# Kernel optimization log

Hardware: AMD Instinct MI355X
Metric: run time of the kernel (lower is better)

## Reference

```python
import jax, jax.numpy as jnp
import numpy as np

B, S, BERT_H = 8, 512, 432
NL, HD = 12, 64
H = NL * HD  # 768
NEG = -1e12

def _lin(k, i, o):
    return jax.random.normal(k, (i, o), jnp.float32) * 0.02

def setup_inputs():
    key = jax.random.key(0)
    ks = jax.random.split(key, 12)
    return {
        "bert_hidden": jax.random.normal(ks[0], (B, S, BERT_H), jnp.float32),
        "attention_mask": jnp.ones((B, S), jnp.float32),
        "dense_w": _lin(ks[1], BERT_H, H), "dense_b": jnp.zeros((H,)),
        "sat_qw": _lin(ks[2], H, H), "sat_qb": jnp.zeros((H,)),
        "sat_kw": _lin(ks[3], H, H), "sat_kb": jnp.zeros((H,)),
        "sat_vw": _lin(ks[4], H, H), "sat_vb": jnp.zeros((H,)),
        "sat_ow": _lin(ks[5], H, H), "sat_ob": jnp.zeros((H,)),
        "rel_qw": _lin(ks[6], H, H), "rel_qb": jnp.zeros((H,)),
        "rel_kw": _lin(ks[7], H, H), "rel_kb": jnp.zeros((H,)),
        "rel_vw": _lin(ks[8], H, H), "rel_vb": jnp.zeros((H,)),
        "rel_ow": _lin(ks[9], H, H), "rel_ob": jnp.zeros((H,)),
        "lns_w": jnp.ones((H,)), "lns_b": jnp.zeros((H,)),
        "lnr_w": jnp.ones((H,)), "lnr_b": jnp.zeros((H,)),
        "head_w": _lin(ks[10], H, 2 * HD), "head_b": jnp.zeros((2 * HD,)),
        "tail_w": _lin(ks[11], 2 * HD, 2 * NL), "tail_b": jnp.zeros((2 * NL,)),
    }

def _layernorm(x, w, b, eps=1e-12):
    u = x.mean(-1, keepdims=True)
    s = ((x - u) ** 2).mean(-1, keepdims=True)
    return w * (x - u) / jnp.sqrt(s + eps) + b

def _mha(q_in, k_in, v_in, wq, bq, wk, bk, wv, bv, wo, bo):
    # q_in: [N, Lq, H]; k_in/v_in: [N, Lk, H]; dropout is identity (eval)
    N, Lq, _ = q_in.shape
    Lk = k_in.shape[1]
    qh = (q_in @ wq + bq).reshape(N, Lq, NL, HD)
    kh = (k_in @ wk + bk).reshape(N, Lk, NL, HD)
    vh = (v_in @ wv + bv).reshape(N, Lk, NL, HD)
    scores = jnp.einsum('nqhd,nkhd->nhqk', qh, kh) / np.float32(np.sqrt(HD))
    probs = jax.nn.softmax(scores, axis=-1)
    ctx = jnp.einsum('nhqk,nkhd->nqhd', probs, vh).reshape(N, Lq, NL * HD)
    return ctx @ wo + bo + q_in

def _shift_back(x):
    # faithful torch cycle_shift(forward=False): circular roll left by 1
    return jnp.roll(x, -1, axis=1)

def _shift_fwd(x):
    # faithful to the torch sequential in-place loop in cycle_shift(forward=True):
    # out[0] = x[-1]; out[1:] = x[0] (each copy reads the already-overwritten slot)
    b, s, h = x.shape
    return jnp.concatenate([x[:, -1:, :], jnp.broadcast_to(x[:, :1, :], (b, s - 1, h))], axis=1)

def reference(bert_hidden, attention_mask, dense_w, dense_b,
              sat_qw, sat_qb, sat_kw, sat_kb, sat_vw, sat_vb, sat_ow, sat_ob,
              rel_qw, rel_qb, rel_kw, rel_kb, rel_vw, rel_vb, rel_ow, rel_ob,
              lns_w, lns_b, lnr_w, lnr_b, head_w, head_b, tail_w, tail_b):
    hidden0 = bert_hidden @ dense_w + dense_b  # [B,S,H]
    cs = hidden0
    center = cs.mean(axis=1)  # [B,H], avg_pool2d over seq dim
    for _ in range(2):
        before = _shift_back(cs)
        after = _shift_fwd(cs)
        center_exp = jnp.broadcast_to(center[:, None, :], cs.shape)
        concats = jnp.stack([before, cs, after, hidden0, center_exp], axis=2)  # [B,S,5,H]
        concats = concats.reshape(B * S, 5, H)
        q = cs.reshape(B * S, 1, H)
        sat = _mha(q, concats, concats, sat_qw, sat_qb, sat_kw, sat_kb, sat_vw, sat_vb, sat_ow, sat_ob)
        cs = _layernorm(jax.nn.relu(sat), lns_w, lns_b).reshape(B, S, H)
        cc = jnp.concatenate([center[:, None, :], cs], axis=1)  # [B,S+1,H]
        rel = _mha(center[:, None, :], cc, cc, rel_qw, rel_qb, rel_kw, rel_kb, rel_vw, rel_vb, rel_ow, rel_ob)
        center = _layernorm(jax.nn.relu(rel), lnr_w, lnr_b)[:, 0, :]
    outputs = cs @ head_w + head_b  # [B,S,2*HD]
    qw, kw = outputs[..., ::2], outputs[..., 1::2]  # [B,S,HD]
    pos = jnp.arange(S, dtype=jnp.float32)
    inv = jnp.power(10000.0, -2.0 * jnp.arange(HD // 2, dtype=jnp.float32) / HD)
    ang = pos[:, None] * inv[None, :]  # [S,HD//2]
    pe = jnp.stack([jnp.sin(ang), jnp.cos(ang)], axis=-1).reshape(S, HD)
    cos_pos = jnp.repeat(pe[:, 1::2], 2, axis=-1)  # [S,HD]
    sin_pos = jnp.repeat(pe[:, ::2], 2, axis=-1)
    def rot(x):
        x2 = jnp.stack([-x[..., 1::2], x[..., ::2]], axis=-1).reshape(x.shape)
        return x * cos_pos + x2 * sin_pos
    qw, kw = rot(qw), rot(kw)
    logits = jnp.einsum('bmd,bnd->bmn', qw, kw) / np.float32(np.sqrt(HD))  # [B,S,S]
    bias = jnp.einsum('bnh->bhn', outputs @ tail_w + tail_b) / 2.0  # [B,2*NL,S]
    logits = logits[:, None, :, :] + bias[:, ::2, None, :] + bias[:, 1::2, :, None]  # [B,NL,S,S]
    m1 = attention_mask[:, None, :, None]
    logits = logits * m1 + NEG * (1.0 - m1)
    m2 = attention_mask[:, None, None, :]
    logits = logits * m2 + NEG * (1.0 - m2)
    tril = jnp.tril(jnp.ones((S, S), logits.dtype), k=-1)
    return logits - tril * 1e12
```

## Files before the change

kernel.cpp:

```cpp
#include <hip/hip_runtime.h>
#include <cstdint>
#include <cstddef>

#define HH 768
#define SS 512
#define NBATCH 8
#define NLH 12
#define HDIM 64
#define BSROWS 4096
static constexpr float NEGV = -1000000000000.0f;

typedef unsigned short ushort_t;
typedef __attribute__((ext_vector_type(4))) float fx4;
typedef __attribute__((ext_vector_type(8))) short sx8;

__device__ __forceinline__ ushort_t f2bf(float f) {
  uint32_t u = __float_as_uint(f);
  uint32_t r = (u + 0x7FFFu + ((u >> 16) & 1u)) >> 16;
  return (ushort_t)r;
}
__device__ __forceinline__ float bf2f(ushort_t h) {
  return __uint_as_float(((uint32_t)h) << 16);
}
__device__ __forceinline__ float2 ldbf2(const ushort_t* p) {
  uint32_t u = *(const uint32_t*)p;
  return make_float2(__uint_as_float(u << 16), __uint_as_float(u & 0xffff0000u));
}

__device__ __forceinline__ void async_copy16(void* lds, const void* g) {
  __builtin_amdgcn_global_load_lds(
      (const __attribute__((address_space(1))) void*)g,
      (__attribute__((address_space(3))) void*)lds, 16, 0, 0);
}

__global__ __launch_bounds__(256) void gemm_bf16(
    const ushort_t* __restrict__ A, int lda,
    const ushort_t* __restrict__ B, int ldb,
    const float* __restrict__ bias,
    const ushort_t* __restrict__ resb,
    ushort_t* __restrict__ Cb, int ldo,
    ushort_t* __restrict__ Cb2, int ldo2, int nsplit, int K, int nx,
    float* __restrict__ colmean)
{
  __shared__ ushort_t As[128 * 64];
  __shared__ ushort_t Bs[128 * 64];
  const int tid = threadIdx.x;
  const int nwg = gridDim.x;
  const int q = nwg >> 3;
  const int xcd = blockIdx.x & 7, sidx = blockIdx.x >> 3;
  const int swz = xcd * q + sidx;
  const int bm = (swz / nx) * 128;
  const int bn = (swz % nx) * 128;
  const int l = tid & 63;
  const int w = tid >> 6;
  const int wr = w >> 1, wc = w & 1;
  const int r8 = tid >> 3;
  const int sl = tid & 7;

  fx4 acc[4][4];
#pragma unroll
  for (int m = 0; m < 4; ++m)
#pragma unroll
    for (int n = 0; n < 4; ++n) acc[m][n] = (fx4)0.f;

  for (int k0 = 0; k0 < K; k0 += 64) {
#pragma unroll
    for (int i = 0; i < 4; ++i) {
      int row = i * 32 + r8;
      int srcs = sl ^ (row & 7);
      async_copy16((char*)As + i * 4096 + tid * 16,
                   A + (size_t)(bm + row) * lda + k0 + srcs * 8);
    }
#pragma unroll
    for (int i = 0; i < 4; ++i) {
      int row = i * 32 + r8;
      int srcs = sl ^ (row & 7);
      async_copy16((char*)Bs + i * 4096 + tid * 16,
                   B + (size_t)(bn + row) * ldb + k0 + srcs * 8);
    }
    __syncthreads();
#pragma unroll
    for (int kk = 0; kk < 2; ++kk) {
      sx8 av[4], bv[4];
      const int so = (l >> 4) + kk * 4;
#pragma unroll
      for (int m = 0; m < 4; ++m) {
        int r = wr * 64 + m * 16 + (l & 15);
        av[m] = *(const sx8*)((const char*)As + r * 128 + ((so ^ (r & 7)) * 16));
      }
#pragma unroll
      for (int n = 0; n < 4; ++n) {
        int r = wc * 64 + n * 16 + (l & 15);
        bv[n] = *(const sx8*)((const char*)Bs + r * 128 + ((so ^ (r & 7)) * 16));
      }
#pragma unroll
      for (int m = 0; m < 4; ++m)
#pragma unroll
        for (int n = 0; n < 4; ++n)
          acc[m][n] = __builtin_amdgcn_mfma_f32_16x16x32_bf16(av[m], bv[n], acc[m][n], 0, 0, 0);
    }
    __syncthreads();
  }

  const bool second = (bn >= nsplit);
  ushort_t* dst = second ? Cb2 : Cb;
  const int ld = second ? ldo2 : ldo;
  const int csub = second ? nsplit : 0;
  const int cr0 = bm + wr * 64 + (l >> 4) * 4;
  const int cc0 = bn + wc * 64 + (l & 15);
#pragma unroll
  for (int m = 0; m < 4; ++m) {
#pragma unroll
    for (int n = 0; n < 4; ++n) {
      int col = cc0 + n * 16;
      float bcol = bias[col];
#pragma unroll
      for (int j = 0; j < 4; ++j) {
        int row = cr0 + m * 16 + j;
        size_t off = (size_t)row * ld + (col - csub);
        float v = acc[m][n][j] + bcol;
        if (resb) v += bf2f(resb[off]);
        dst[off] = f2bf(v);
      }
    }
  }

  if (colmean) {
    float* scr = (float*)As;
    const int cid = wr * 4 + (l >> 4);
#pragma unroll
    for (int n = 0; n < 4; ++n) {
      int colL = wc * 64 + n * 16 + (l & 15);
      float t = 16.0f * bias[bn + colL];
#pragma unroll
      for (int m = 0; m < 4; ++m)
#pragma unroll
        for (int j = 0; j < 4; ++j) t += acc[m][n][j];
      scr[cid * 128 + colL] = t;
    }
    __syncthreads();
    if (tid < 128) {
      float scol = 0.f;
#pragma unroll
      for (int c = 0; c < 8; ++c) scol += scr[c * 128 + tid];
      atomicAdd(&colmean[(bm >> 9) * HH + bn + tid], scol * (1.0f / 512.0f));
    }
  }
}

__global__ __launch_bounds__(256) void head_fused(
    const ushort_t* __restrict__ A,
    const ushort_t* __restrict__ B,
    const float* __restrict__ head_b,
    const float* __restrict__ tail_w,
    const float* __restrict__ tail_b,
    float* __restrict__ qw, float* __restrict__ kw,
    float* __restrict__ bias2)
{
  __shared__ ushort_t As[128 * 64];
  __shared__ ushort_t Bs[128 * 64];
  __shared__ float tile[128][130];
  __shared__ float invt[32];
  const int tid = threadIdx.x;
  const int bm = blockIdx.x * 128;
  const int l = tid & 63;
  const int w = tid >> 6;
  const int wr = w >> 1, wc = w & 1;
  const int r8 = tid >> 3;
  const int sl = tid & 7;

  if (tid < 32) invt[tid] = powf(10000.0f, -(float)tid / 32.0f);

  fx4 acc[4][4];
#pragma unroll
  for (int m = 0; m < 4; ++m)
#pragma unroll
    for (int n = 0; n < 4; ++n) acc[m][n] = (fx4)0.f;

  for (int k0 = 0; k0 < HH; k0 += 64) {
#pragma unroll
    for (int i = 0; i < 4; ++i) {
      int row = i * 32 + r8;
      int srcs = sl ^ (row & 7);
      async_copy16((char*)As + i * 4096 + tid * 16,
                   A + (size_t)(bm + row) * HH + k0 + srcs * 8);
    }
#pragma unroll
    for (int i = 0; i < 4; ++i) {
      int row = i * 32 + r8;
      int srcs = sl ^ (row & 7);
      async_copy16((char*)Bs + i * 4096 + tid * 16,
                   B + (size_t)row * HH + k0 + srcs * 8);
    }
    __syncthreads();
#pragma unroll
    for (int kk = 0; kk < 2; ++kk) {
      sx8 av[4], bv[4];
      const int so = (l >> 4) + kk * 4;
#pragma unroll
      for (int m = 0; m < 4; ++m) {
        int r = wr * 64 + m * 16 + (l & 15);
        av[m] = *(const sx8*)((const char*)As + r * 128 + ((so ^ (r & 7)) * 16));
      }
#pragma unroll
      for (int n = 0; n < 4; ++n) {
        int r = wc * 64 + n * 16 + (l & 15);
        bv[n] = *(const sx8*)((const char*)Bs + r * 128 + ((so ^ (r & 7)) * 16));
      }
#pragma unroll
      for (int m = 0; m < 4; ++m)
#pragma unroll
        for (int n = 0; n < 4; ++n)
          acc[m][n] = __builtin_amdgcn_mfma_f32_16x16x32_bf16(av[m], bv[n], acc[m][n], 0, 0, 0);
    }
    __syncthreads();
  }

  const int cr0 = wr * 64 + (l >> 4) * 4;
  const int cc0 = wc * 64 + (l & 15);
#pragma unroll
  for (int m = 0; m < 4; ++m)
#pragma unroll
    for (int n = 0; n < 4; ++n) {
      int col = cc0 + n * 16;
      float bcol = head_b[col];
#pragma unroll
      for (int j = 0; j < 4; ++j)
        tile[cr0 + m * 16 + j][col] = acc[m][n][j] + bcol;
    }
  __syncthreads();

  for (int t = tid; t < 128 * 32; t += 256) {
    int r = t >> 5, i = t & 31;
    int s = (bm + r) & 511;
    float ang = (float)s * invt[i];
    float sn = sinf(ang), cn = cosf(ang);
    float q0 = tile[r][4 * i + 0], k0 = tile[r][4 * i + 1];
    float q1 = tile[r][4 * i + 2], k1 = tile[r][4 * i + 3];
    float* qp = qw + (size_t)(bm + r) * 64 + i * 2;
    float* kp = kw + (size_t)(bm + r) * 64 + i * 2;
    qp[0] = q0 * cn - q1 * sn; qp[1] = q1 * cn + q0 * sn;
    kp[0] = k0 * cn - k1 * sn; kp[1] = k1 * cn + k0 * sn;
  }
  for (int t = tid; t < 128 * 24; t += 256) {
    int r = t / 24, c = t % 24;
    float acc2 = tail_b[c];
// ... 28 lines not shown
    }
    __syncthreads();
#pragma unroll
    for (int i = 0; i < 4; ++i) {
      int n = n0 + ty + i * 8;
      int k = k0 + tx;
      if (n < jb.N && k < jb.Kpad)
        jb.dst[(size_t)(jb.rowOff + n) * jb.Kpad + k] = f2bf(t[tx][ty + i * 8]);
    }
  } else {
    const int NB = BSROWS * 448;
    const int total = NB + 3840 + NBATCH * HH;
    int start = (blockIdx.y * 24 + blockIdx.x) * 256 + threadIdx.x;
    for (int i = start; i < total; i += 24 * 24 * 256) {
      if (i < NB) {
        int r = i / 448, c = i % 448;
        pa.bert_bf[i] = (c < 432) ? f2bf(pa.bert[(size_t)r * 432 + c]) : (ushort_t)0;
      } else if (i < NB + 3840) {
        int c = i - NB;
        float v;
        if (c < 768) v = pa.rkb[c];
        else if (c < 1536) v = pa.rvb[c - 768];
        else if (c < 2304) v = pa.sqb[c - 1536];
        else if (c < 3072) v = pa.skb[c - 2304];
        else v = pa.svb[c - 3072];
        pa.b_merged[c] = v;
      } else {
        pa.center[i - NB - 3840] = 0.f;
      }
    }
  }
}

struct SmallJob { const float* W; const float* bias; const float* res; float* C; };
struct SmallJobs { SmallJob j[5]; };
__global__ __launch_bounds__(256) void gemm_skinny(
    const float* __restrict__ A, SmallJobs jobs)
{
  __shared__ float As[8 * HH];
  __shared__ float part[8 * 8 * 32];
  const int tid = threadIdx.x;
  const SmallJob job = jobs.j[blockIdx.y];
#pragma unroll
  for (int i = 0; i < 6; ++i) {
    int idx = tid * 4 + i * 1024;
    *(float4*)&As[idx] = *(const float4*)(A + idx);
  }
  __syncthreads();
  const int c = tid & 31;
  const int col = (blockIdx.x << 5) + c;
  const int ks = tid >> 5;
  const float* Wp = job.W + (size_t)(ks * 96) * HH + col;
  float acc[8] = {};
#pragma unroll 8
  for (int k = 0; k < 96; ++k) {
    float wv = Wp[(size_t)k * HH];
    const float* ap = &As[ks * 96 + k];
#pragma unroll
    for (int m = 0; m < 8; ++m)
      acc[m] = fmaf(ap[m * HH], wv, acc[m]);
  }
#pragma unroll
  for (int m = 0; m < 8; ++m)
    part[ks * 256 + m * 32 + c] = acc[m];
  __syncthreads();
  const int m = tid >> 5;
  const int c2 = tid & 31;
  float s = 0.f;
#pragma unroll
  for (int k = 0; k < 8; ++k) s += part[k * 256 + m * 32 + c2];
  const int outcol = (blockIdx.x << 5) + c2;
  float v = s + job.bias[outcol];
  if (job.res) v += job.res[(size_t)m * HH + outcol];
  job.C[(size_t)m * HH + outcol] = v;
}

struct SmallJobs2 { SmallJob j[2]; };
__global__ __launch_bounds__(256) void skinny_ln(
    const float* __restrict__ relo, const float* __restrict__ lw, const float* __restrict__ lb,
    SmallJobs2 jobs)
{
  __shared__ float As[8 * HH];
  __shared__ float part[8 * 8 * 32];
  const int tid = threadIdx.x;
  const SmallJob job = jobs.j[blockIdx.y];
#pragma unroll
  for (int i = 0; i < 6; ++i) {
    int idx = tid * 4 + i * 1024;
    *(float4*)&As[idx] = *(const float4*)(relo + idx);
  }
  __syncthreads();
  {
    const int row = tid >> 5, lc = tid & 31;
    float s = 0.f, sq = 0.f;
#pragma unroll
    for (int e = 0; e < 24; ++e) {
      float x = fmaxf(As[row * HH + lc * 24 + e], 0.f);
      s += x; sq += x * x;
    }
#pragma unroll
    for (int d = 1; d < 32; d <<= 1) { s += __shfl_xor(s, d); sq += __shfl_xor(sq, d); }
    float mean = s * (1.0f / HH);
    float var = sq * (1.0f / HH) - mean * mean;
    float rstd = rsqrtf(var + 1e-12f);
#pragma unroll
    for (int e = 0; e < 24; ++e) {
      int cc = lc * 24 + e;
      float x = fmaxf(As[row * HH + cc], 0.f);
      As[row * HH + cc] = lw[cc] * (x - mean) * rstd + lb[cc];
    }
  }
  __syncthreads();
  const int c = tid & 31;
  const int col = (blockIdx.x << 5) + c;
  const int ks = tid >> 5;
  const float* Wp = job.W + (size_t)(ks * 96) * HH + col;
  float acc[8] = {};
#pragma unroll 8
  for (int k = 0; k < 96; ++k) {
    float wv = Wp[(size_t)k * HH];
    const float* ap = &As[ks * 96 + k];
#pragma unroll
    for (int m = 0; m < 8; ++m)
      acc[m] = fmaf(ap[m * HH], wv, acc[m]);
  }
#pragma unroll
  for (int m = 0; m < 8; ++m)
    part[ks * 256 + m * 32 + c] = acc[m];
  __syncthreads();
  const int m = tid >> 5;
  const int c2 = tid & 31;
  float s2 = 0.f;
#pragma unroll
  for (int k = 0; k < 8; ++k) s2 += part[k * 256 + m * 32 + c2];
  const int outcol = (blockIdx.x << 5) + c2;
  job.C[(size_t)m * HH + outcol] = s2 + job.bias[outcol];
}

__global__ __launch_bounds__(256) void sat_attn(
    const ushort_t* __restrict__ Qc, const ushort_t* __restrict__ Kc,
    const ushort_t* __restrict__ Vc, int ldq,
    const ushort_t* __restrict__ Kh0, const ushort_t* __restrict__ Vh0, int ldh,
    const float* __restrict__ Kcen, const float* __restrict__ Vcen,
    ushort_t* __restrict__ ctxb)
{
  int i = blockIdx.x;
  int b = i >> 9, s = i & 511;
  int lane = threadIdx.x & 63;
  int wave = threadIdx.x >> 6;
  size_t rb = (size_t)(b * SS + ((s + 1) & 511));
  size_t rs = (size_t)i;
  size_t ra = (size_t)(b * SS + (s == 0 ? (SS - 1) : 0));
  size_t rc = (size_t)b * HH;
  const int half = lane >> 5;
  const int d0 = (lane & 31) * 2;
#pragma unroll
  for (int it = 0; it < 2; ++it) {
    int p = wave + 4 * it;
    if (p >= 6) break;
    int off = (2 * p + half) * HDIM + d0;
    float2 q  = ldbf2(Qc + rs * ldq + off);
    float2 kb = ldbf2(Kc + rb * ldq + off);
    float2 ks = ldbf2(Kc + rs * ldq + off);
    float2 ka = ldbf2(Kc + ra * ldq + off);
    float2 kh = ldbf2(Kh0 + rs * ldh + off);
    float2 kc = *(const float2*)(Kcen + rc + off);
    float s0 = q.x * kb.x + q.y * kb.y;
    float s1 = q.x * ks.x + q.y * ks.y;
    float s2 = q.x * ka.x + q.y * ka.y;
    float s3 = q.x * kh.x + q.y * kh.y;
    float s4 = q.x * kc.x + q.y * kc.y;
// ... 21 lines not shown
}

__global__ __launch_bounds__(256) void relu_ln_bf(
    const ushort_t* __restrict__ x, const float* __restrict__ w, const float* __restrict__ b,
    ushort_t* __restrict__ ybf)
{
  int row = blockIdx.x;
  const ushort_t* xr = x + (size_t)row * HH;
  float v[3];
  float sum = 0.f, sumsq = 0.f;
#pragma unroll
  for (int j = 0; j < 3; ++j) {
    float t = bf2f(xr[threadIdx.x + j * 256]);
    t = fmaxf(t, 0.f);
    v[j] = t;
    sum += t; sumsq += t * t;
  }
#pragma unroll
  for (int d = 1; d < 64; d <<= 1) { sum += __shfl_xor(sum, d); sumsq += __shfl_xor(sumsq, d); }
  __shared__ float ws_[4], wsq_[4];
  int wave = threadIdx.x >> 6, lane = threadIdx.x & 63;
  if (lane == 0) { ws_[wave] = sum; wsq_[wave] = sumsq; }
  __syncthreads();
  sum = ws_[0] + ws_[1] + ws_[2] + ws_[3];
  sumsq = wsq_[0] + wsq_[1] + wsq_[2] + wsq_[3];
  float mean = sum * (1.0f / HH);
  float var = sumsq * (1.0f / HH) - mean * mean;
  float rstd = rsqrtf(var + 1e-12f);
#pragma unroll
  for (int j = 0; j < 3; ++j) {
    int cidx = threadIdx.x + j * 256;
    float o = w[cidx] * (v[j] - mean) * rstd + b[cidx];
    ybf[(size_t)row * HH + cidx] = f2bf(o);
  }
}

__global__ __launch_bounds__(256) void rel_attn(
    const float* __restrict__ Qr, const float* __restrict__ Krc, const ushort_t* __restrict__ Kr,
    const float* __restrict__ Vrc, const ushort_t* __restrict__ Vr, int ldkv,
    float* __restrict__ ctx)
{
  int b = blockIdx.x, h = blockIdx.y;
  __shared__ float qs[64];
  __shared__ float sc[513];
  __shared__ float part[4][64];
  __shared__ float redm[4], redsum[4];
  int t = threadIdx.x, lane = t & 63, wave = t >> 6;
  if (t < 64) qs[t] = Qr[b * HH + h * HDIM + t];
  __syncthreads();
  for (int j = t; j < 513; j += 256) {
    float acc = 0.f;
    if (j == 0) {
      const float* kp = Krc + b * HH + h * HDIM;
#pragma unroll
      for (int d = 0; d < HDIM; ++d) acc = fmaf(qs[d], kp[d], acc);
    } else {
      const sx8* kv = (const sx8*)(Kr + (size_t)(b * SS + j - 1) * ldkv + h * HDIM);
#pragma unroll
      for (int dq = 0; dq < 8; ++dq) {
        sx8 v = kv[dq];
#pragma unroll
        for (int e = 0; e < 8; ++e)
          acc = fmaf(qs[dq * 8 + e], bf2f((ushort_t)v[e]), acc);
      }
    }
    sc[j] = acc * 0.125f;
  }
  __syncthreads();
  float m = -1e30f;
  for (int j = t; j < 513; j += 256) m = fmaxf(m, sc[j]);
#pragma unroll
  for (int d = 1; d < 64; d <<= 1) m = fmaxf(m, __shfl_xor(m, d));
  if (lane == 0) redm[wave] = m;
  __syncthreads();
  m = fmaxf(fmaxf(redm[0], redm[1]), fmaxf(redm[2], redm[3]));
  float lsum = 0.f;
  for (int j = t; j < 513; j += 256) { float e = __expf(sc[j] - m); sc[j] = e; lsum += e; }
#pragma unroll
  for (int d = 1; d < 64; d <<= 1) lsum += __shfl_xor(lsum, d);
  if (lane == 0) redsum[wave] = lsum;
  __syncthreads();
  float total = redsum[0] + redsum[1] + redsum[2] + redsum[3];
  float accv = 0.f;
#pragma unroll 8
  for (int j = wave; j < 513; j += 4) {
    float vv = (j == 0) ? Vrc[b * HH + h * HDIM + lane]
                        : bf2f(Vr[(size_t)(b * SS + j - 1) * ldkv + h * HDIM + lane]);
    accv = fmaf(sc[j], vv, accv);
  }
  part[wave][lane] = accv;
  __syncthreads();
  if (wave == 0) {
    float r = (part[0][lane] + part[1][lane] + part[2][lane] + part[3][lane]) / total;
    ctx[b * HH + h * HDIM + lane] = r;
  }
}

__global__ __launch_bounds__(256) void final_kernel(
    const float* __restrict__ qw, const float* __restrict__ kw,
    const float* __restrict__ bias2, const float* __restrict__ mask,
    float* __restrict__ out)
{
  int b = blockIdx.z;
  int mt = blockIdx.y * 32;
  int nt = blockIdx.x * 32;
  __shared__ float qs[32][68];
  __shared__ float ks[32][68];
  int t = threadIdx.x;
  {
    int idx = t * 8;
    int r = idx >> 6, c = idx & 63;
    const float* sq = qw + (size_t)(b * SS + mt + r) * 64 + c;
    const float* sk = kw + (size_t)(b * SS + nt + r) * 64 + c;
    *(float4*)&qs[r][c]     = *(const float4*)(sq);
    *(float4*)&qs[r][c + 4] = *(const float4*)(sq + 4);
    *(float4*)&ks[r][c]     = *(const float4*)(sk);
    *(float4*)&ks[r][c + 4] = *(const float4*)(sk + 4);
  }
  __syncthreads();
  int m = t >> 3;
  int n0 = (t & 7) * 4;
  float d0 = 0.f, d1 = 0.f, d2 = 0.f, d3 = 0.f;
#pragma unroll
  for (int d = 0; d < 64; d += 4) {
    float4 qv = *(const float4*)&qs[m][d];
    float4 k0 = *(const float4*)&ks[n0 + 0][d];
    float4 k1 = *(const float4*)&ks[n0 + 1][d];
// ... 60 lines not shown
  const float* rel_vw  = (const float*)d_in[16];
  const float* rel_vb  = (const float*)d_in[17];
  const float* rel_ow  = (const float*)d_in[18];
  const float* rel_ob  = (const float*)d_in[19];
  const float* lns_w   = (const float*)d_in[20];
  const float* lns_b   = (const float*)d_in[21];
  const float* lnr_w   = (const float*)d_in[22];
  const float* lnr_b   = (const float*)d_in[23];
  const float* head_w  = (const float*)d_in[24];
  const float* head_b  = (const float*)d_in[25];
  const float* tail_w  = (const float*)d_in[26];
  const float* tail_b  = (const float*)d_in[27];

  float* out = (float*)d_out;
  char*  ws  = (char*)d_ws;

  size_t off = 0;
  auto alloc = [&](size_t bytes) { char* p = ws + off; off += (bytes + 255) & ~(size_t)255; return p; };
  ushort_t* bert_bf   = (ushort_t*)alloc((size_t)BSROWS * 448 * 2);
  ushort_t* Wt_dense  = (ushort_t*)alloc((size_t)768 * 448 * 2);
  ushort_t* Wt_big    = (ushort_t*)alloc((size_t)3840 * 768 * 2);
  ushort_t* Wt_satow  = (ushort_t*)alloc((size_t)768 * 768 * 2);
  ushort_t* Wt_head   = (ushort_t*)alloc((size_t)128 * 768 * 2);
  ushort_t* hidden0_bf= (ushort_t*)alloc((size_t)BSROWS * HH * 2);
  ushort_t* ctx_bf    = (ushort_t*)alloc((size_t)BSROWS * HH * 2);
  ushort_t* csA_bf    = (ushort_t*)alloc((size_t)BSROWS * HH * 2);
  float* b_merged = (float*)alloc(3840 * 4);
  float* center   = (float*)alloc(6144 * 4);
  float* Kcen     = (float*)alloc(6144 * 4);
  float* Vcen     = (float*)alloc(6144 * 4);
  float* Qr       = (float*)alloc(6144 * 4);
  float* Krc      = (float*)alloc(6144 * 4);
  float* Vrc      = (float*)alloc(6144 * 4);
  float* ctxr     = (float*)alloc(6144 * 4);
  float* relo     = (float*)alloc(6144 * 4);
  float* bias2    = (float*)alloc((size_t)BSROWS * 24 * 4);
  float* qwbuf    = (float*)alloc((size_t)BSROWS * 64 * 4);
  float* kwbuf    = (float*)alloc((size_t)BSROWS * 64 * 4);

  ushort_t* QKV1_bf = (ushort_t*)out;
  ushort_t* tmp1_bf = QKV1_bf + (size_t)BSROWS * 2304;
  ushort_t* KrVr_bf = tmp1_bf + (size_t)BSROWS * 768;
  ushort_t* QKV2_bf = KrVr_bf + (size_t)BSROWS * 1536;
  ushort_t* tmp2_bf = tmp1_bf;

  dim3 blk(256);

  {
    PrepArgs pa;
    pa.j[0] = { dense_w, Wt_dense, 432, 768, 448, 0 };
    pa.j[1] = { rel_kw,  Wt_big,   768, 768, 768, 0 };
    pa.j[2] = { rel_vw,  Wt_big,   768, 768, 768, 768 };
    pa.j[3] = { sat_qw,  Wt_big,   768, 768, 768, 1536 };
    pa.j[4] = { sat_kw,  Wt_big,   768, 768, 768, 2304 };
    pa.j[5] = { sat_vw,  Wt_big,   768, 768, 768, 3072 };
    pa.j[6] = { sat_ow,  Wt_satow, 768, 768, 768, 0 };
    pa.j[7] = { head_w,  Wt_head,  768, 128, 768, 0 };
    pa.bert = bert; pa.bert_bf = bert_bf;
    pa.rkb = rel_kb; pa.rvb = rel_vb; pa.sqb = sat_qb; pa.skb = sat_kb; pa.svb = sat_vb;
    pa.b_merged = b_merged; pa.center = center;
    prep_all<<<dim3(24, 24, 9), blk, 0, stream>>>(pa);
  }

  gemm_bf16<<<dim3(192), blk, 0, stream>>>(bert_bf, 448, Wt_dense, 448, dense_b,
                                           nullptr, hidden0_bf, HH,
                                           nullptr, 0, 1 << 30, 448, 6, center);

  gemm_bf16<<<dim3(576), blk, 0, stream>>>(hidden0_bf, HH, Wt_big + (size_t)1536 * 768, HH,
                                           b_merged + 1536, nullptr, QKV1_bf, 2304,
                                           nullptr, 0, 1 << 30, HH, 18, nullptr);
  {
    SmallJobs jobs;
    jobs.j[0] = { sat_kw, sat_kb, nullptr, Kcen };
    jobs.j[1] = { sat_vw, sat_vb, nullptr, Vcen };
    jobs.j[2] = { rel_qw, rel_qb, nullptr, Qr };
    jobs.j[3] = { rel_kw, rel_kb, nullptr, Krc };
    jobs.j[4] = { rel_vw, rel_vb, nullptr, Vrc };
    gemm_skinny<<<dim3(24, 5), blk, 0, stream>>>(center, jobs);
  }
  sat_attn<<<BSROWS, 256, 0, stream>>>(QKV1_bf, QKV1_bf + 768, QKV1_bf + 1536, 2304,
                                       QKV1_bf + 768, QKV1_bf + 1536, 2304,
                                       Kcen, Vcen, ctx_bf);
  gemm_bf16<<<dim3(192), blk, 0, stream>>>(ctx_bf, HH, Wt_satow, HH, sat_ob,
                                           hidden0_bf, tmp1_bf, HH,
                                           nullptr, 0, 1 << 30, HH, 6, nullptr);
  relu_ln_bf<<<BSROWS, 256, 0, stream>>>(tmp1_bf, lns_w, lns_b, csA_bf);

  gemm_bf16<<<dim3(960), blk, 0, stream>>>(csA_bf, HH, Wt_big, HH, b_merged,
                                           nullptr, KrVr_bf, 1536,
                                           QKV2_bf, 2304, 1536, HH, 30, nullptr);
  rel_attn<<<dim3(8, 12), 256, 0, stream>>>(Qr, Krc, KrVr_bf, Vrc, KrVr_bf + 768, 1536, ctxr);
  {
    SmallJobs jobs;
    jobs.j[0] = { rel_ow, rel_ob, center, relo };
    gemm_skinny<<<dim3(24, 1), blk, 0, stream>>>(ctxr, jobs);
  }
  {
    SmallJobs2 jobs;
    jobs.j[0] = { sat_kw, sat_kb, nullptr, Kcen };
    jobs.j[1] = { sat_vw, sat_vb, nullptr, Vcen };
    skinny_ln<<<dim3(24, 2), blk, 0, stream>>>(relo, lnr_w, lnr_b, jobs);
  }
  sat_attn<<<BSROWS, 256, 0, stream>>>(QKV2_bf, QKV2_bf + 768, QKV2_bf + 1536, 2304,
                                       QKV1_bf + 768, QKV1_bf + 1536, 2304,
                                       Kcen, Vcen, ctx_bf);
  gemm_bf16<<<dim3(192), blk, 0, stream>>>(ctx_bf, HH, Wt_satow, HH, sat_ob,
                                           csA_bf, tmp2_bf, HH,
                                           nullptr, 0, 1 << 30, HH, 6, nullptr);
  relu_ln_bf<<<BSROWS, 256, 0, stream>>>(tmp2_bf, lns_w, lns_b, csA_bf);

  head_fused<<<32, blk, 0, stream>>>(csA_bf, Wt_head, head_b, tail_w, tail_b,
                                     qwbuf, kwbuf, bias2);
  final_kernel<<<dim3(16, 16, 8), 256, 0, stream>>>(qwbuf, kwbuf, bias2, amask, out);
}
```

Measured before the change: 311.8 us.

## Fuse small kernels: QKV GEMM with skinny jobs, relation chain, and final LN into head

Three separate fusions. The QKV1 GEMM and the skinny center projections now run in one launch with block-index dispatch. The relation attention, output projection, ReLU-LayerNorm and K/V center projections are merged into a single 1024-thread kernel per batch. The last relu_ln pass is folded into head_fused, which computes row statistics up front and normalizes the A tile while loading it. This removes several launches and intermediate round trips, but rel_fused runs on only 8 blocks with serial fp32 GEMV loops, and the head LN loads A synchronously instead of asynchronously.

```diff
diff --git a/kernel.cpp b/kernel.cpp
--- a/kernel.cpp
+++ b/kernel.cpp
@@ -31,6 +31,166 @@
   __builtin_amdgcn_global_load_lds(
       (const __attribute__((address_space(1))) void*)g,
       (__attribute__((address_space(3))) void*)lds, 16, 0, 0);
+}
+
+__device__ __forceinline__ void gemm_core(
+    char* arena, int bid, int nwg, int nx,
+    const ushort_t* __restrict__ A, int lda,
+    const ushort_t* __restrict__ B, int ldb,
+    const float* __restrict__ bias,
+    const ushort_t* __restrict__ resb,
+    ushort_t* __restrict__ Cb, int ldo,
+    ushort_t* __restrict__ Cb2, int ldo2, int nsplit, int K,
+    float* __restrict__ colmean)
+{
+  ushort_t* As = (ushort_t*)arena;
+  ushort_t* Bs = (ushort_t*)(arena + 16384);
+  const int tid = threadIdx.x;
+  const int q = nwg >> 3;
+  const int xcd = bid & 7, sidx = bid >> 3;
+  const int swz = xcd * q + sidx;
+  const int bm = (swz / nx) * 128;
+  const int bn = (swz % nx) * 128;
+  const int l = tid & 63;
+  const int w = tid >> 6;
+  const int wr = w >> 1, wc = w & 1;
+  const int r8 = tid >> 3;
+  const int sl = tid & 7;
+
+  fx4 acc[4][4];
+#pragma unroll
+  for (int m = 0; m < 4; ++m)
+#pragma unroll
+    for (int n = 0; n < 4; ++n) acc[m][n] = (fx4)0.f;
+
+  for (int k0 = 0; k0 < K; k0 += 64) {
+#pragma unroll
+    for (int i = 0; i < 4; ++i) {
+      int row = i * 32 + r8;
+      int srcs = sl ^ (row & 7);
+      async_copy16((char*)As + i * 4096 + tid * 16,
+                   A + (size_t)(bm + row) * lda + k0 + srcs * 8);
+    }
+#pragma unroll
+    for (int i = 0; i < 4; ++i) {
+      int row = i * 32 + r8;
+      int srcs = sl ^ (row & 7);
+      async_copy16((char*)Bs + i * 4096 + tid * 16,
+                   B + (size_t)(bn + row) * ldb + k0 + srcs * 8);
+    }
+    __syncthreads();
+#pragma unroll
+    for (int kk = 0; kk < 2; ++kk) {
+      sx8 av[4], bv[4];
+      const int so = (l >> 4) + kk * 4;
+#pragma unroll
+      for (int m = 0; m < 4; ++m) {
+        int r = wr * 64 + m * 16 + (l & 15);
+        av[m] = *(const sx8*)((const char*)As + r * 128 + ((so ^ (r & 7)) * 16));
+      }
+#pragma unroll
+      for (int n = 0; n < 4; ++n) {
+        int r = wc * 64 + n * 16 + (l & 15);
+        bv[n] = *(const sx8*)((const char*)Bs + r * 128 + ((so ^ (r & 7)) * 16));
+      }
+#pragma unroll
+      for (int m = 0; m < 4; ++m)
+#pragma unroll
+        for (int n = 0; n < 4; ++n)
+          acc[m][n] = __builtin_amdgcn_mfma_f32_16x16x32_bf16(av[m], bv[n], acc[m][n], 0, 0, 0);
+    }
+    __syncthreads();
+  }
+
+  const bool second = (bn >= nsplit);
+  ushort_t* dst = second ? Cb2 : Cb;
+  const int ld = second ? ldo2 : ldo;
+  const int csub = second ? nsplit : 0;
+  const int cr0 = bm + wr * 64 + (l >> 4) * 4;
+  const int cc0 = bn + wc * 64 + (l & 15);
+#pragma unroll
+  for (int m = 0; m < 4; ++m) {
+#pragma unroll
+    for (int n = 0; n < 4; ++n) {
+      int col = cc0 + n * 16;
+      float bcol = bias[col];
+#pragma unroll
+      for (int j = 0; j < 4; ++j) {
+        int row = cr0 + m * 16 + j;
+        size_t off = (size_t)row * ld + (col - csub);
+        float v = acc[m][n][j] + bcol;
+        if (resb) v += bf2f(resb[off]);
+        dst[off] = f2bf(v);
+      }
+    }
+  }
+
+  if (colmean) {
+    float* scr = (float*)arena;
+    const int cid = wr * 4 + (l >> 4);
+#pragma unroll
+    for (int n = 0; n < 4; ++n) {
+      int colL = wc * 64 + n * 16 + (l & 15);
+      float t = 16.0f * bias[bn + colL];
+#pragma unroll
+      for (int m = 0; m < 4; ++m)
+#pragma unroll
+        for (int j = 0; j < 4; ++j) t += acc[m][n][j];
+      scr[cid * 128 + colL] = t;
+    }
+    __syncthreads();
+    if (tid < 128) {
+      float scol = 0.f;
+#pragma unroll
+      for (int c = 0; c < 8; ++c) scol += scr[c * 128 + tid];
+      atomicAdd(&colmean[(bm >> 9) * HH + bn + tid], scol * (1.0f / 512.0f));
+    }
+  }
+}
+
+struct SmallJob { const float* W; const float* bias; const float* res; float* C; };
+struct SmallJobs { SmallJob j[5]; };
+
+__device__ __forceinline__ void skinny_core(
+    char* arena, int colblk,
+    const float* __restrict__ A, const float* __restrict__ W,
+    const float* __restrict__ bias, const float* __restrict__ res, float* __restrict__ C)
+{
+  float* As = (float*)arena;
+  float* part = (float*)(arena + 24576);
+  const int tid = threadIdx.x;
+#pragma unroll
+  for (int i = 0; i < 6; ++i) {
+    int idx = tid * 4 + i * 1024;
+    *(float4*)&As[idx] = *(const float4*)(A + idx);
+  }
+  __syncthreads();
+  const int c = tid & 31;
+  const int col = (colblk << 5) + c;
+  const int ks = tid >> 5;
+  const float* Wp = W + (size_t)(ks * 96) * HH + col;
+  float acc[8] = {};
+#pragma unroll 8
+  for (int k = 0; k < 96; ++k) {
+    float wv = Wp[(size_t)k * HH];
+    const float* ap = &As[ks * 96 + k];
+#pragma unroll
+    for (int m = 0; m < 8; ++m)
+      acc[m] = fmaf(ap[m * HH], wv, acc[m]);
+  }
+#pragma unroll
+  for (int m = 0; m < 8; ++m)
+    part[ks * 256 + m * 32 + c] = acc[m];
+  __syncthreads();
+  const int m = tid >> 5;
+  const int c2 = tid & 31;
+  float s = 0.f;
+#pragma unroll
+  for (int k = 0; k < 8; ++k) s += part[k * 256 + m * 32 + c2];
+  const int outcol = (colblk << 5) + c2;
+  float v = s + bias[outcol];
+  if (res) v += res[(size_t)m * HH + outcol];
+  C[(size_t)m * HH + outcol] = v;
 }
 
 __global__ __launch_bounds__(256) void gemm_bf16(
@@ -42,114 +202,159 @@
     ushort_t* __restrict__ Cb2, int ldo2, int nsplit, int K, int nx,
     float* __restrict__ colmean)
 {
-  __shared__ ushort_t As[128 * 64];
-  __shared__ ushort_t Bs[128 * 64];
+  __shared__ char arena[32768];
+  gemm_core(arena, blockIdx.x, gridDim.x, nx, A, lda, B, ldb, bias, resb,
+            Cb, ldo, Cb2, ldo2, nsplit, K, colmean);
+}
+
+__global__ __launch_bounds__(256) void qkv_center(
+    const ushort_t* __restrict__ A, const ushort_t* __restrict__ B,
+    const float* __restrict__ bias, ushort_t* __restrict__ Cb,
+    SmallJobs jobs, const float* __restrict__ center)
+{
+  __shared__ char arena[32768];
+  if (blockIdx.x < 576) {
+    gemm_core(arena, blockIdx.x, 576, 18, A, HH, B, HH, bias, nullptr,
+              Cb, 2304, nullptr, 0, 1 << 30, HH, nullptr);
+  } else {
+    int vb = blockIdx.x - 576;
+    SmallJob jb = jobs.j[vb / 24];
+    skinny_core(arena, vb % 24, center, jb.W, jb.bias, jb.res, jb.C);
+  }
+}
+
+__global__ __launch_bounds__(1024) void rel_fused(
+    const float* __restrict__ Qr, const float* __restrict__ Krc,
+    const float* __restrict__ Vrc, const ushort_t* __restrict__ KrVr,
+    const float* __restrict__ center,
+    const float* __restrict__ rel_ow, const float* __restrict__ rel_ob,
+    const float* __restrict__ lnr_w, const float* __restrict__ lnr_b,
+    const float* __restrict__ sat_kw, const float* __restrict__ sat_kb,
+    const float* __restrict__ sat_vw, const float* __restrict__ sat_vb,
+    float* __restrict__ Kcen, float* __restrict__ Vcen)
+{
+  const int b = blockIdx.x;
   const int tid = threadIdx.x;
-  const int nwg = gridDim.x;
-  const int q = nwg >> 3;
-  const int xcd = blockIdx.x & 7, sidx = blockIdx.x >> 3;
-  const int swz = xcd * q + sidx;
-  const int bm = (swz / nx) * 128;
-  const int bn = (swz % nx) * 128;
-  const int l = tid & 63;
-  const int w = tid >> 6;
-  const int wr = w >> 1, wc = w & 1;
-  const int r8 = tid >> 3;
-  const int sl = tid & 7;
-
-  fx4 acc[4][4];
-#pragma unroll
-  for (int m = 0; m < 4; ++m)
-#pragma unroll
-    for (int n = 0; n < 4; ++n) acc[m][n] = (fx4)0.f;
-
-  for (int k0 = 0; k0 < K; k0 += 64) {
-#pragma unroll
-    for (int i = 0; i < 4; ++i) {
-      int row = i * 32 + r8;
-      int srcs = sl ^ (row & 7);
-      async_copy16((char*)As + i * 4096 + tid * 16,
-                   A + (size_t)(bm + row) * lda + k0 + srcs * 8);
-    }
-#pragma unroll
-    for (int i = 0; i < 4; ++i) {
-      int row = i * 32 + r8;
-      int srcs = sl ^ (row & 7);
-      async_copy16((char*)Bs + i * 4096 + tid * 16,
-                   B + (size_t)(bn + row) * ldb + k0 + srcs * 8);
-    }
+  __shared__ float sc[12][513];
+  __shared__ float qrow[768];
+  __shared__ float part[3072];
+  __shared__ float ctxrow[768];
+  __shared__ float relorow[768];
+  __shared__ float red[34];
+
+  if (tid < 768) qrow[tid] = Qr[b * HH + tid];
+  __syncthreads();
+
+  for (int idx = tid; idx < 12 * 513; idx += 1024) {
+    int h = idx / 513, j = idx - h * 513;
+    float acc = 0.f;
+    if (j == 0) {
+      const float* kp = Krc + b * HH + h * HDIM;
+#pragma unroll
+      for (int d = 0; d < HDIM; ++d) acc = fmaf(qrow[h * HDIM + d], kp[d], acc);
+    } else {
+      const sx8* kv = (const sx8*)(KrVr + (size_t)(b * SS + j - 1) * 1536 + h * HDIM);
+#pragma unroll
+      for (int dq = 0; dq < 8; ++dq) {
+        sx8 v = kv[dq];
+#pragma unroll
+        for (int e = 0; e < 8; ++e)
+          acc = fmaf(qrow[h * HDIM + dq * 8 + e], bf2f((ushort_t)v[e]), acc);
+      }
+    }
+    sc[h][j] = acc * 0.125f;
+  }
+  __syncthreads();
+
+  {
+    int h = tid >> 6, lane = tid & 63;
+    if (h < 12) {
+      float m = -1e30f;
+      for (int j = lane; j < 513; j += 64) m = fmaxf(m, sc[h][j]);
+#pragma unroll
+      for (int d = 1; d < 64; d <<= 1) m = fmaxf(m, __shfl_xor(m, d));
+      float s = 0.f;
+      for (int j = lane; j < 513; j += 64) {
+        float e = __expf(sc[h][j] - m);
+        sc[h][j] = e; s += e;
+      }
+#pragma unroll
+      for (int d = 1; d < 64; d <<= 1) s += __shfl_xor(s, d);
+      float inv = 1.f / s;
+      for (int j = lane; j < 513; j += 64) sc[h][j] *= inv;
+    }
+  }
+  __syncthreads();
+
+  for (int idx = tid; idx < 3072; idx += 1024) {
+    int jq = idx & 3, od = idx >> 2;
+    int h = od >> 6, d = od & 63;
+    float acc = 0.f;
+    int j = jq;
+    if (jq == 0) { acc = sc[h][0] * Vrc[b * HH + h * HDIM + d]; j = 4; }
+    for (; j < 513; j += 4)
+      acc = fmaf(sc[h][j],
+                 bf2f(KrVr[(size_t)(b * SS + j - 1) * 1536 + 768 + h * HDIM + d]), acc);
+    part[idx] = acc;
+  }
+  __syncthreads();
+  if (tid < 768)
+    ctxrow[tid] = part[4 * tid] + part[4 * tid + 1] + part[4 * tid + 2] + part[4 * tid + 3];
+  __syncthreads();
+
+  if (tid < 768) {
+    float a0 = 0.f, a1 = 0.f, a2 = 0.f, a3 = 0.f;
+    for (int k = 0; k < 768; k += 4) {
+      a0 = fmaf(ctxrow[k + 0], rel_ow[(size_t)(k + 0) * HH + tid], a0);
+      a1 = fmaf(ctxrow[k + 1], rel_ow[(size_t)(k + 1) * HH + tid], a1);
+      a2 = fmaf(ctxrow[k + 2], rel_ow[(size_t)(k + 2) * HH + tid], a2);
+      a3 = fmaf(ctxrow[k + 3], rel_ow[(size_t)(k + 3) * HH + tid], a3);
+    }
+    relorow[tid] = (a0 + a1) + (a2 + a3) + rel_ob[tid] + center[b * HH + tid];
+  }
+  __syncthreads();
+
+  {
+    float x = (tid < 768) ? fmaxf(relorow[tid], 0.f) : 0.f;
+    float s = x, sq = x * x;
+#pragma unroll
+    for (int d = 1; d < 64; d <<= 1) { s += __shfl_xor(s, d); sq += __shfl_xor(sq, d); }
+    if ((tid & 63) == 0) { red[tid >> 6] = s; red[16 + (tid >> 6)] = sq; }
     __syncthreads();
-#pragma unroll
-    for (int kk = 0; kk < 2; ++kk) {
-      sx8 av[4], bv[4];
-      const int so = (l >> 4) + kk * 4;
-#pragma unroll
-      for (int m = 0; m < 4; ++m) {
-        int r = wr * 64 + m * 16 + (l & 15);
-        av[m] = *(const sx8*)((const char*)As + r * 128 + ((so ^ (r & 7)) * 16));
-      }
-#pragma unroll
-      for (int n = 0; n < 4; ++n) {
-        int r = wc * 64 + n * 16 + (l & 15);
-        bv[n] = *(const sx8*)((const char*)Bs + r * 128 + ((so ^ (r & 7)) * 16));
-      }
-#pragma unroll
-      for (int m = 0; m < 4; ++m)
-#pragma unroll
-        for (int n = 0; n < 4; ++n)
-          acc[m][n] = __builtin_amdgcn_mfma_f32_16x16x32_bf16(av[m], bv[n], acc[m][n], 0, 0, 0);
+    if (tid == 0) {
+      float S = 0.f, SQ = 0.f;
+#pragma unroll
+      for (int wv = 0; wv < 16; ++wv) { S += red[wv]; SQ += red[16 + wv]; }
+      float mean = S * (1.0f / HH);
+      float var = SQ * (1.0f / HH) - mean * mean;
+      red[32] = mean;
+      red[33] = rsqrtf(var + 1e-12f);
     }
     __syncthreads();
-  }
-
-  const bool second = (bn >= nsplit);
-  ushort_t* dst = second ? Cb2 : Cb;
-  const int ld = second ? ldo2 : ldo;
-  const int csub = second ? nsplit : 0;
-  const int cr0 = bm + wr * 64 + (l >> 4) * 4;
-  const int cc0 = bn + wc * 64 + (l & 15);
-#pragma unroll
-  for (int m = 0; m < 4; ++m) {
-#pragma unroll
-    for (int n = 0; n < 4; ++n) {
-      int col = cc0 + n * 16;
-      float bcol = bias[col];
-#pragma unroll
-      for (int j = 0; j < 4; ++j) {
-        int row = cr0 + m * 16 + j;
-        size_t off = (size_t)row * ld + (col - csub);
-        float v = acc[m][n][j] + bcol;
-        if (resb) v += bf2f(resb[off]);
-        dst[off] = f2bf(v);
-      }
-    }
-  }
-
-  if (colmean) {
-    float* scr = (float*)As;
-    const int cid = wr * 4 + (l >> 4);
-#pragma unroll
-    for (int n = 0; n < 4; ++n) {
-      int colL = wc * 64 + n * 16 + (l & 15);
-      float t = 16.0f * bias[bn + colL];
-#pragma unroll
-      for (int m = 0; m < 4; ++m)
-#pragma unroll
-        for (int j = 0; j < 4; ++j) t += acc[m][n][j];
-      scr[cid * 128 + colL] = t;
-    }
-    __syncthreads();
-    if (tid < 128) {
-      float scol = 0.f;
-#pragma unroll
-      for (int c = 0; c < 8; ++c) scol += scr[c * 128 + tid];
-      atomicAdd(&colmean[(bm >> 9) * HH + bn + tid], scol * (1.0f / 512.0f));
-    }
+    if (tid < 768)
+      relorow[tid] = lnr_w[tid] * (fmaxf(relorow[tid], 0.f) - red[32]) * red[33] + lnr_b[tid];
+  }
+  __syncthreads();
+
+  for (int idx = tid; idx < 1536; idx += 1024) {
+    const bool isv = idx >= 768;
+    int col = isv ? idx - 768 : idx;
+    const float* W = isv ? sat_vw : sat_kw;
+    float a0 = 0.f, a1 = 0.f, a2 = 0.f, a3 = 0.f;
+    for (int k = 0; k < 768; k += 4) {
+      a0 = fmaf(relorow[k + 0], W[(size_t)(k + 0) * HH + col], a0);
+      a1 = fmaf(relorow[k + 1], W[(size_t)(k + 1) * HH + col], a1);
+      a2 = fmaf(relorow[k + 2], W[(size_t)(k + 2) * HH + col], a2);
+      a3 = fmaf(relorow[k + 3], W[(size_t)(k + 3) * HH + col], a3);
+    }
+    float v = (a0 + a1) + (a2 + a3) + (isv ? sat_vb[col] : sat_kb[col]);
+    (isv ? Vcen : Kcen)[b * HH + col] = v;
   }
 }
 
 __global__ __launch_bounds__(256) void head_fused(
-    const ushort_t* __restrict__ A,
+    const ushort_t* __restrict__ Araw,
+    const float* __restrict__ lnw, const float* __restrict__ lnb,
     const ushort_t* __restrict__ B,
     const float* __restrict__ head_b,
     const float* __restrict__ tail_w,
@@ -161,6 +366,7 @@
   __shared__ ushort_t Bs[128 * 64];
   __shared__ float tile[128][130];
   __shared__ float invt[32];
+  __shared__ float2 rst[128];
   const int tid = threadIdx.x;
   const int bm = blockIdx.x * 128;
   const int l = tid & 63;
@@ -171,6 +377,28 @@
 
   if (tid < 32) invt[tid] = powf(10000.0f, -(float)tid / 32.0f);
 
+  {
+    int row = tid >> 1, half = tid & 1;
+    const ushort_t* rp = Araw + (size_t)(bm + row) * HH + half * 384;
+    float s = 0.f, sq = 0.f;
+#pragma unroll 8
+    for (int c = 0; c < 48; ++c) {
+      sx8 v = *(const sx8*)(rp + c * 8);
+#pragma unroll
+      for (int e = 0; e < 8; ++e) {
+        float x = fmaxf(bf2f((ushort_t)v[e]), 0.f);
+        s += x; sq += x * x;
+      }
+    }
+    s += __shfl_xor(s, 1); sq += __shfl_xor(sq, 1);
+    if (half == 0) {
+      float mean = s * (1.0f / HH);
+      float var = sq * (1.0f / HH) - mean * mean;
+      rst[row] = make_float2(mean, rsqrtf(var + 1e-12f));
+    }
+  }
+  __syncthreads();
+
   fx4 acc[4][4];
 #pragma unroll
   for (int m = 0; m < 4; ++m)
@@ -178,13 +406,6 @@
     for (int n = 0; n < 4; ++n) acc[m][n] = (fx4)0.f;
 
   for (int k0 = 0; k0 < HH; k0 += 64) {
-#pragma unroll
-    for (int i = 0; i < 4; ++i) {
-      int row = i * 32 + r8;
-      int srcs = sl ^ (row & 7);
-      async_copy16((char*)As + i * 4096 + tid * 16,
-                   A + (size_t)(bm + row) * HH + k0 + srcs * 8);
-    }
 #pragma unroll
     for (int i = 0; i < 4; ++i) {
       int row = i * 32 + r8;
@@ -192,10 +413,31 @@
       async_copy16((char*)Bs + i * 4096 + tid * 16,
                    B + (size_t)row * HH + k0 + srcs * 8);
     }
+#pragma unroll
+    for (int i = 0; i < 4; ++i) {
+      int row = i * 32 + r8;
+      int slot = sl ^ (row & 7);
+      int gk = k0 + slot * 8;
+      sx8 v = *(const sx8*)(Araw + (size_t)(bm + row) * HH + gk);
+      float4 w0 = *(const float4*)(lnw + gk);
+      float4 w1 = *(const float4*)(lnw + gk + 4);
+      float4 b0 = *(const float4*)(lnb + gk);
+      float4 b1 = *(const float4*)(lnb + gk + 4);
+      float wv[8] = {w0.x, w0.y, w0.z, w0.w, w1.x, w1.y, w1.z, w1.w};
+      float bv[8] = {b0.x, b0.y, b0.z, b0.w, b1.x, b1.y, b1.z, b1.w};
+      float2 mr = rst[row];
+      sx8 ov;
+#pragma unroll
+      for (int e = 0; e < 8; ++e) {
+        float x = fmaxf(bf2f((ushort_t)v[e]), 0.f);
+        ov[e] = (short)f2bf(fmaf((x - mr.x) * mr.y, wv[e], bv[e]));
+      }
+      *(sx8*)((char*)As + i * 4096 + tid * 16) = ov;
+    }
     __syncthreads();
 #pragma unroll
     for (int kk = 0; kk < 2; ++kk) {
-      sx8 av[4], bv[4];
+      sx8 av[4], bvv[4];
       const int so = (l >> 4) + kk * 4;
 #pragma unroll
       for (int m = 0; m < 4; ++m) {
@@ -205,13 +447,13 @@
 #pragma unroll
       for (int n = 0; n < 4; ++n) {
         int r = wc * 64 + n * 16 + (l & 15);
-        bv[n] = *(const sx8*)((const char*)Bs + r * 128 + ((so ^ (r & 7)) * 16));
+        bvv[n] = *(const sx8*)((const char*)Bs + r * 128 + ((so ^ (r & 7)) * 16));
       }
 #pragma unroll
       for (int m = 0; m < 4; ++m)
 #pragma unroll
         for (int n = 0; n < 4; ++n)
-          acc[m][n] = __builtin_amdgcn_mfma_f32_16x16x32_bf16(av[m], bv[n], acc[m][n], 0, 0, 0);
+          acc[m][n] = __builtin_amdgcn_mfma_f32_16x16x32_bf16(av[m], bvv[n], acc[m][n], 0, 0, 0);
     }
     __syncthreads();
   }
@@ -306,111 +548,6 @@
   }
 }
 
-struct SmallJob { const float* W; const float* bias; const float* res; float* C; };
-struct SmallJobs { SmallJob j[5]; };
-__global__ __launch_bounds__(256) void gemm_skinny(
-    const float* __restrict__ A, SmallJobs jobs)
-{
-  __shared__ float As[8 * HH];
-  __shared__ float part[8 * 8 * 32];
-  const int tid = threadIdx.x;
-  const SmallJob job = jobs.j[blockIdx.y];
-#pragma unroll
-  for (int i = 0; i < 6; ++i) {
-    int idx = tid * 4 + i * 1024;
-    *(float4*)&As[idx] = *(const float4*)(A + idx);
-  }
-  __syncthreads();
-  const int c = tid & 31;
-  const int col = (blockIdx.x << 5) + c;
-  const int ks = tid >> 5;
-  const float* Wp = job.W + (size_t)(ks * 96) * HH + col;
-  float acc[8] = {};
-#pragma unroll 8
-  for (int k = 0; k < 96; ++k) {
-    float wv = Wp[(size_t)k * HH];
-    const float* ap = &As[ks * 96 + k];
-#pragma unroll
-    for (int m = 0; m < 8; ++m)
-      acc[m] = fmaf(ap[m * HH], wv, acc[m]);
-  }
-#pragma unroll
-  for (int m = 0; m < 8; ++m)
-    part[ks * 256 + m * 32 + c] = acc[m];
-  __syncthreads();
-  const int m = tid >> 5;
-  const int c2 = tid & 31;
-  float s = 0.f;
-#pragma unroll
-  for (int k = 0; k < 8; ++k) s += part[k * 256 + m * 32 + c2];
-  const int outcol = (blockIdx.x << 5) + c2;
-  float v = s + job.bias[outcol];
-  if (job.res) v += job.res[(size_t)m * HH + outcol];
-  job.C[(size_t)m * HH + outcol] = v;
-}
-
-struct SmallJobs2 { SmallJob j[2]; };
-__global__ __launch_bounds__(256) void skinny_ln(
-    const float* __restrict__ relo, const float* __restrict__ lw, const float* __restrict__ lb,
-    SmallJobs2 jobs)
-{
-  __shared__ float As[8 * HH];
-  __shared__ float part[8 * 8 * 32];
-  const int tid = threadIdx.x;
-  const SmallJob job = jobs.j[blockIdx.y];
-#pragma unroll
-  for (int i = 0; i < 6; ++i) {
-    int idx = tid * 4 + i * 1024;
-    *(float4*)&As[idx] = *(const float4*)(relo + idx);
-  }
-  __syncthreads();
-  {
-    const int row = tid >> 5, lc = tid & 31;
-    float s = 0.f, sq = 0.f;
-#pragma unroll
-    for (int e = 0; e < 24; ++e) {
-      float x = fmaxf(As[row * HH + lc * 24 + e], 0.f);
-      s += x; sq += x * x;
-    }
-#pragma unroll
-    for (int d = 1; d < 32; d <<= 1) { s += __shfl_xor(s, d); sq += __shfl_xor(sq, d); }
-    float mean = s * (1.0f / HH);
-    float var = sq * (1.0f / HH) - mean * mean;
-    float rstd = rsqrtf(var + 1e-12f);
-#pragma unroll
-    for (int e = 0; e < 24; ++e) {
-      int cc = lc * 24 + e;
-      float x = fmaxf(As[row * HH + cc], 0.f);
-      As[row * HH + cc] = lw[cc] * (x - mean) * rstd + lb[cc];
-    }
-  }
-  __syncthreads();
-  const int c = tid & 31;
-  const int col = (blockIdx.x << 5) + c;
-  const int ks = tid >> 5;
-  const float* Wp = job.W + (size_t)(ks * 96) * HH + col;
-  float acc[8] = {};
-#pragma unroll 8
-  for (int k = 0; k < 96; ++k) {
-    float wv = Wp[(size_t)k * HH];
-    const float* ap = &As[ks * 96 + k];
-#pragma unroll
-    for (int m = 0; m < 8; ++m)
-      acc[m] = fmaf(ap[m * HH], wv, acc[m]);
-  }
-#pragma unroll
-  for (int m = 0; m < 8; ++m)
-    part[ks * 256 + m * 32 + c] = acc[m];
-  __syncthreads();
-  const int m = tid >> 5;
-  const int c2 = tid & 31;
-  float s2 = 0.f;
-#pragma unroll
-  for (int k = 0; k < 8; ++k) s2 += part[k * 256 + m * 32 + c2];
-  const int outcol = (blockIdx.x << 5) + c2;
-  job.C[(size_t)m * HH + outcol] = s2 + job.bias[outcol];
-}
-
 __global__ __launch_bounds__(256) void sat_attn(
     const ushort_t* __restrict__ Qc, const ushort_t* __restrict__ Kc,
     const ushort_t* __restrict__ Vc, int ldq,
@@ -498,67 +635,6 @@
     int cidx = threadIdx.x + j * 256;
     float o = w[cidx] * (v[j] - mean) * rstd + b[cidx];
     ybf[(size_t)row * HH + cidx] = f2bf(o);
-  }
-}
-
-__global__ __launch_bounds__(256) void rel_attn(
-    const float* __restrict__ Qr, const float* __restrict__ Krc, const ushort_t* __restrict__ Kr,
-    const float* __restrict__ Vrc, const ushort_t* __restrict__ Vr, int ldkv,
-    float* __restrict__ ctx)
-{
-  int b = blockIdx.x, h = blockIdx.y;
-  __shared__ float qs[64];
-  __shared__ float sc[513];
-  __shared__ float part[4][64];
-  __shared__ float redm[4], redsum[4];
-  int t = threadIdx.x, lane = t & 63, wave = t >> 6;
-  if (t < 64) qs[t] = Qr[b * HH + h * HDIM + t];
-  __syncthreads();
-  for (int j = t; j < 513; j += 256) {
-    float acc = 0.f;
-    if (j == 0) {
-      const float* kp = Krc + b * HH + h * HDIM;
-#pragma unroll
-      for (int d = 0; d < HDIM; ++d) acc = fmaf(qs[d], kp[d], acc);
-    } else {
-      const sx8* kv = (const sx8*)(Kr + (size_t)(b * SS + j - 1) * ldkv + h * HDIM);
-#pragma unroll
-      for (int dq = 0; dq < 8; ++dq) {
-        sx8 v = kv[dq];
-#pragma unroll
-        for (int e = 0; e < 8; ++e)
-          acc = fmaf(qs[dq * 8 + e], bf2f((ushort_t)v[e]), acc);
-      }
-    }
-    sc[j] = acc * 0.125f;
-  }
-  __syncthreads();
-  float m = -1e30f;
-  for (int j = t; j < 513; j += 256) m = fmaxf(m, sc[j]);
-#pragma unroll
-  for (int d = 1; d < 64; d <<= 1) m = fmaxf(m, __shfl_xor(m, d));
-  if (lane == 0) redm[wave] = m;
-  __syncthreads();
-  m = fmaxf(fmaxf(redm[0], redm[1]), fmaxf(redm[2], redm[3]));
-  float lsum = 0.f;
-  for (int j = t; j < 513; j += 256) { float e = __expf(sc[j] - m); sc[j] = e; lsum += e; }
-#pragma unroll
-  for (int d = 1; d < 64; d <<= 1) lsum += __shfl_xor(lsum, d);
-  if (lane == 0) redsum[wave] = lsum;
-  __syncthreads();
-  float total = redsum[0] + redsum[1] + redsum[2] + redsum[3];
-  float accv = 0.f;
-#pragma unroll 8
-  for (int j = wave; j < 513; j += 4) {
-    float vv = (j == 0) ? Vrc[b * HH + h * HDIM + lane]
-                        : bf2f(Vr[(size_t)(b * SS + j - 1) * ldkv + h * HDIM + lane]);
-    accv = fmaf(sc[j], vv, accv);
-  }
-  part[wave][lane] = accv;
-  __syncthreads();
-  if (wave == 0) {
-    float r = (part[0][lane] + part[1][lane] + part[2][lane] + part[3][lane]) / total;
-    ctx[b * HH + h * HDIM + lane] = r;
   }
 }
 
@@ -685,8 +761,6 @@
   float* Qr       = (float*)alloc(6144 * 4);
   float* Krc      = (float*)alloc(6144 * 4);
   float* Vrc      = (float*)alloc(6144 * 4);
-  float* ctxr     = (float*)alloc(6144 * 4);
-  float* relo     = (float*)alloc(6144 * 4);
   float* bias2    = (float*)alloc((size_t)BSROWS * 24 * 4);
   float* qwbuf    = (float*)alloc((size_t)BSROWS * 64 * 4);
   float* kwbuf    = (float*)alloc((size_t)BSROWS * 64 * 4);
@@ -719,9 +793,6 @@
                                            nullptr, hidden0_bf, HH,
                                            nullptr, 0, 1 << 30, 448, 6, center);
 
-  gemm_bf16<<<dim3(576), blk, 0, stream>>>(hidden0_bf, HH, Wt_big + (size_t)1536 * 768, HH,
-                                           b_merged + 1536, nullptr, QKV1_bf, 2304,
-                                           nullptr, 0, 1 << 30, HH, 18, nullptr);
   {
     SmallJobs jobs;
     jobs.j[0] = { sat_kw, sat_kb, nullptr, Kcen };
@@ -729,7 +800,8 @@
     jobs.j[2] = { rel_qw, rel_qb, nullptr, Qr };
     jobs.j[3] = { rel_kw, rel_kb, nullptr, Krc };
     jobs.j[4] = { rel_vw, rel_vb, nullptr, Vrc };
-    gemm_skinny<<<dim3(24, 5), blk, 0, stream>>>(center, jobs);
+    qkv_center<<<dim3(696), blk, 0, stream>>>(hidden0_bf, Wt_big + (size_t)1536 * 768,
+                                              b_merged + 1536, QKV1_bf, jobs, center);
   }
   sat_attn<<<BSROWS, 256, 0, stream>>>(QKV1_bf, QKV1_bf + 768, QKV1_bf + 1536, 2304,
                                        QKV1_bf + 768, QKV1_bf + 1536, 2304,
@@ -742,27 +814,17 @@
   gemm_bf16<<<dim3(960), blk, 0, stream>>>(csA_bf, HH, Wt_big, HH, b_merged,
                                            nullptr, KrVr_bf, 1536,
                                            QKV2_bf, 2304, 1536, HH, 30, nullptr);
-  rel_attn<<<dim3(8, 12), 256, 0, stream>>>(Qr, Krc, KrVr_bf, Vrc, KrVr_bf + 768, 1536, ctxr);
-  {
-    SmallJobs jobs;
-    jobs.j[0] = { rel_ow, rel_ob, center, relo };
-    gemm_skinny<<<dim3(24, 1), blk, 0, stream>>>(ctxr, jobs);
-  }
-  {
-    SmallJobs2 jobs;
-    jobs.j[0] = { sat_kw, sat_kb, nullptr, Kcen };
-    jobs.j[1] = { sat_vw, sat_vb, nullptr, Vcen };
-    skinny_ln<<<dim3(24, 2), blk, 0, stream>>>(relo, lnr_w, lnr_b, jobs);
-  }
+  rel_fused<<<dim3(8), dim3(1024), 0, stream>>>(Qr, Krc, Vrc, KrVr_bf, center,
+                                                rel_ow, rel_ob, lnr_w, lnr_b,
+                                                sat_kw, sat_kb, sat_vw, sat_vb,
+                                                Kcen, Vcen);
   sat_attn<<<BSROWS, 256, 0, stream>>>(QKV2_bf, QKV2_bf + 768, QKV2_bf + 1536, 2304,
                                        QKV1_bf + 768, QKV1_bf + 1536, 2304,
                                        Kcen, Vcen, ctx_bf);
   gemm_bf16<<<dim3(192), blk, 0, stream>>>(ctx_bf, HH, Wt_satow, HH, sat_ob,
                                            csA_bf, tmp2_bf, HH,
                                            nullptr, 0, 1 << 30, HH, 6, nullptr);
-  relu_ln_bf<<<BSROWS, 256, 0, stream>>>(tmp2_bf, lns_w, lns_b, csA_bf);
-
-  head_fused<<<32, blk, 0, stream>>>(csA_bf, Wt_head, head_b, tail_w, tail_b,
-                                     qwbuf, kwbuf, bias2);
+  head_fused<<<32, blk, 0, stream>>>(tmp2_bf, lns_w, lns_b, Wt_head, head_b,
+                                     tail_w, tail_b, qwbuf, kwbuf, bias2);
   final_kernel<<<dim3(16, 16, 8), 256, 0, stream>>>(qwbuf, kwbuf, bias2, amask, out);
 }
```

Measured after the change: 504.3 us. 61.8% more time.
